# Kernel optimization log

Measured on AMD Instinct MI355X. Metric: run time of the kernel, lower is better.

## Reference

```python
import jax, jax.numpy as jnp
import numpy as np

L = 12      # n_blocks
H = 12      # n_heads
V = 64      # val_dim
D = 768     # hidden_d (token dim)
MLP = 3072  # MLP_dim
NP = 14     # n_patches per side
PS = 16     # patch size
C = 3       # channels
NC = 1000   # num_classes
EPS = 1e-5  # LayerNorm eps


def pos_embeddings(S, d):
    # result[i,j] = sin(i/10000**(j/d)) if j even else cos(i/10000**((j-1)/d))
    i = jnp.arange(S, dtype=jnp.float32)[:, None]
    j = jnp.arange(d, dtype=jnp.float32)[None, :]
    angle = i / jnp.power(10000.0, (j - (j % 2)) / d)
    even = (jnp.arange(d) % 2) == 0
    return jnp.where(even[None, :], jnp.sin(angle), jnp.cos(angle))


def patchify(images):
    # [n,C,H,W] -> [n, NP*NP, C*PS*PS], patch flattened in (c, ph, pw) order
    n = images.shape[0]
    x = images.reshape(n, C, NP, PS, NP, PS)
    x = x.transpose(0, 2, 4, 1, 3, 5)  # n, i, j, c, ps, ps
    return x.reshape(n, NP * NP, C * PS * PS)


def layernorm(x, w, b):
    m = jnp.mean(x, axis=-1, keepdims=True)
    v = jnp.var(x, axis=-1, keepdims=True)
    return (x - m) * jax.lax.rsqrt(v + EPS) * w + b


def setup_inputs() -> dict:
    key = jax.random.key(0)
    ks = jax.random.split(key, 10)
    s = lambda k, shape, scale=0.02: jax.random.normal(k, shape, jnp.float32) * scale
    return {
        "images": jax.random.normal(ks[0], (32, C, NP * PS, NP * PS), jnp.float32),
        "W_map": s(ks[1], (C * PS * PS, D)),          # linear_mapper (no bias)
        "class_token": s(ks[2], (1, D), 1.0),
        "pos_emb": pos_embeddings(NP * NP + 1, D),     # buffer
        "ln1_w": jnp.ones((L, D)), "ln1_b": jnp.zeros((L, D)),
        "qkv_w": s(ks[3], (L, D, 3 * H * V)),          # to_qkv (no bias)
        "merge_w": s(ks[4], (L, H * V, D)),            # Merge (no bias)
        "ln2_w": jnp.ones((L, D)), "ln2_b": jnp.zeros((L, D)),
        "mlp_w1": s(ks[5], (L, D, MLP)), "mlp_b1": jnp.zeros((L, MLP)),
        "mlp_w2": s(ks[6], (L, MLP, D)), "mlp_b2": jnp.zeros((L, D)),
        "head_w": s(ks[7], (D, NC)), "head_b": jnp.zeros((NC,)),
    }


def reference(images, W_map, class_token, pos_emb, ln1_w, ln1_b, qkv_w,
              merge_w, ln2_w, ln2_b, mlp_w1, mlp_b1, mlp_w2, mlp_b2,
              head_w, head_b):
    n = images.shape[0]
    tokens = patchify(images) @ W_map                              # [n, P, D]
    tokens = jnp.concatenate([jnp.broadcast_to(class_token, (n, 1, D)), tokens], axis=1)
    x = tokens + pos_emb                                           # [n, P+1, D]

    def block(x, p):
        l1w, l1b, qw, mw, l2w, l2b, w1, b1, w2, b2 = p
        h = layernorm(x, l1w, l1b)
        # rearrange 'b p (h v k) -> k b h p v' (k innermost factor)
        qkv = (h @ qw).reshape(n, -1, H, V, 3)
        q, k, v = qkv[..., 0], qkv[..., 1], qkv[..., 2]            # [n, P+1, H, V]
        attn = jnp.einsum('bihd,bjhd->bhij', q, k) * (V ** -0.5)
        attn = jax.nn.softmax(attn, axis=-1)
        o = jnp.einsum('bhij,bjhd->bihd', attn, v).reshape(n, -1, H * V)
        x = x + o @ mw
        h2 = layernorm(x, l2w, l2b)
        x = x + (jax.nn.gelu(h2 @ w1 + b1, approximate=False) @ w2 + b2)
        return x, None

    x, _ = jax.lax.scan(block, x, (ln1_w, ln1_b, qkv_w, merge_w,
                                   ln2_w, ln2_b, mlp_w1, mlp_b1, mlp_w2, mlp_b2))
    return jax.nn.softmax(x[:, 0] @ head_w + head_b, axis=-1)      # [n, NC]
```

## Files before the change

### kernel.cpp

```cpp
#include <hip/hip_runtime.h>
#include <math.h>

#define NIMG 32
#define NP2  196
#define PTOK 197
#define DIM  768
#define NH   12
#define VD   64
#define MLPD 3072
#define ROWS (NIMG*PTOK)
#define PROWS (NIMG*NP2)
#define LDK 40
#define PSTR 208
#define BHN (NIMG*NH)

typedef float f32x4 __attribute__((ext_vector_type(4)));
typedef short bf16x8 __attribute__((ext_vector_type(8)));
typedef unsigned short u16x8 __attribute__((ext_vector_type(8)));
typedef unsigned short u16x4 __attribute__((ext_vector_type(4)));

__device__ __forceinline__ unsigned short f2bf(float x) {
    unsigned int u = __float_as_uint(x);
    return (unsigned short)((u + 0x7FFFu + ((u >> 16) & 1u)) >> 16);
}
__device__ __forceinline__ float bfhi(unsigned short h) {
    return __uint_as_float(((unsigned int)h) << 16);
}

__global__ __launch_bounds__(256) void patchify_kernel(const float* __restrict__ img,
                                                       float* __restrict__ out)
{
    int idx = blockIdx.x * 256 + threadIdx.x;
    if (idx >= PROWS * DIM) return;
    int row = idx / DIM, kk = idx % DIM;
    int b = row / NP2, p = row % NP2;
    int i = p / 14, j = p % 14;
    int c = kk >> 8, r = kk & 255;
    int ph = r >> 4, pw = r & 15;
    out[idx] = img[(((size_t)b*3 + c)*224 + i*16 + ph)*224 + j*16 + pw];
}

__global__ __launch_bounds__(256) void class_pos_kernel(const float* __restrict__ ct,
                                                        const float* __restrict__ pos,
                                                        float* __restrict__ x)
{
    int idx = blockIdx.x * 256 + threadIdx.x;
    if (idx >= NIMG * DIM) return;
    int b = idx / DIM, d = idx % DIM;
    x[(size_t)b * PTOK * DIM + d] = ct[d] + pos[d];
}

__device__ __forceinline__ void conv_body(const float* __restrict__ W,
    unsigned short* __restrict__ Bh, unsigned short* __restrict__ Bl, int K, int N)
{
    int idx = blockIdx.x * 256 + threadIdx.x;
    if (idx >= N * (K >> 5)) return;
    int kb = idx / N;
    int n  = idx - kb * N;
    size_t off = (((size_t)(n >> 7) * (K >> 5) + kb) * 128 + (n & 127)) * 32;
    #pragma unroll
    for (int u = 0; u < 4; ++u) {
        u16x8 h, l;
        #pragma unroll
        for (int j = 0; j < 8; ++j) {
            float x = W[(size_t)(kb * 32 + u * 8 + j) * N + n];
            unsigned short hh = f2bf(x);
            h[j] = hh;
            l[j] = f2bf(x - bfhi(hh));
        }
        *(u16x8*)&Bh[off + u * 8] = h;
        *(u16x8*)&Bl[off + u * 8] = l;
    }
}

__global__ __launch_bounds__(256) void convert_one(const float* __restrict__ W,
    unsigned short* __restrict__ Bh, unsigned short* __restrict__ Bl, int K, int N)
{
    conv_body(W, Bh, Bl, K, N);
}

__global__ __launch_bounds__(256) void convert_layer(
    const float* __restrict__ qw, const float* __restrict__ mw,
    const float* __restrict__ w1, const float* __restrict__ w2,
    unsigned short* qh, unsigned short* ql, unsigned short* mh, unsigned short* ml,
    unsigned short* h1, unsigned short* l1, unsigned short* h2, unsigned short* l2)
{
    switch (blockIdx.y) {
        case 0: conv_body(qw, qh, ql, DIM, 3*NH*VD); break;
        case 1: conv_body(mw, mh, ml, DIM, DIM);     break;
        case 2: conv_body(w1, h1, l1, DIM, MLPD);    break;
        case 3: conv_body(w2, h2, l2, MLPD, DIM);    break;
    }
}

template<int MODE>
__global__ __launch_bounds__(256, 2) void mgemm(
    const float* __restrict__ A,
    const unsigned short* __restrict__ Bh, const unsigned short* __restrict__ Bl,
    float* __restrict__ C, int M, int N, int K,
    const float* __restrict__ bias, const float* __restrict__ res,
    const float* __restrict__ pos,
    unsigned int* __restrict__ qo, unsigned int* __restrict__ ko, unsigned int* __restrict__ vo)
{
    __shared__ unsigned short AhS[128 * LDK];
    __shared__ unsigned short AlS[128 * LDK];
    __shared__ unsigned short BhS[128 * LDK];
    __shared__ unsigned short BlS[128 * LDK];

    const int tid = threadIdx.x;
    const int m0 = blockIdx.y * 128, n0 = blockIdx.x * 128;
    const int wave = tid >> 6, lane = tid & 63;
    const int wm = (wave >> 1) * 64, wn = (wave & 1) * 64;
    const int lr = lane & 15, lg = lane >> 4;

    const int ar = tid >> 1, ac = (tid & 1) * 16;
    const bool aok = (m0 + ar) < M;
    const float* aP = A + (size_t)(aok ? (m0 + ar) : 0) * K + ac;
    const size_t bBase = ((size_t)(n0 >> 7) * (K >> 5)) * 4096 + (size_t)tid * 16;
    const unsigned short* bhP = Bh + bBase;
    const unsigned short* blP = Bl + bBase;
    const int wOff = ar * LDK + ac;
    const int aOff = (wm + lr) * LDK + lg * 8;
    const int bOff = (wn + lr) * LDK + lg * 8;

    f32x4 acc[4][4];
    #pragma unroll
    for (int i = 0; i < 4; ++i)
        #pragma unroll
        for (int j = 0; j < 4; ++j)
            #pragma unroll
            for (int e = 0; e < 4; ++e) acc[i][j][e] = 0.f;

    f32x4 avr0, avr1, avr2, avr3;
    u16x8 bhr0, bhr1, blr0, blr1;

#define LOAD_REGS(KS) do { \
    const float* _p = aP + (size_t)(KS) * 32; \
    avr0 = *(const f32x4*)(_p);      avr1 = *(const f32x4*)(_p + 4); \
    avr2 = *(const f32x4*)(_p + 8);  avr3 = *(const f32x4*)(_p + 12); \
    const unsigned short* _ph = bhP + (size_t)(KS) * 4096; \
    const unsigned short* _pl = blP + (size_t)(KS) * 4096; \
    bhr0 = *(const u16x8*)(_ph); bhr1 = *(const u16x8*)(_ph + 8); \
    blr0 = *(const u16x8*)(_pl); blr1 = *(const u16x8*)(_pl + 8); \
} while (0)

    const int kSteps = K >> 5;
    LOAD_REGS(0);

    #pragma unroll 1
    for (int ks = 0; ks < kSteps; ++ks) {
        __syncthreads();
        {
            u16x8 ahv, alv;
            #pragma unroll
            for (int j = 0; j < 4; ++j) {
                unsigned short hh = f2bf(avr0[j]);
                ahv[j] = hh; alv[j] = f2bf(avr0[j] - bfhi(hh));
            }
            #pragma unroll
            for (int j = 0; j < 4; ++j) {
                unsigned short hh = f2bf(avr1[j]);
                ahv[4 + j] = hh; alv[4 + j] = f2bf(avr1[j] - bfhi(hh));
            }
            *(u16x8*)&AhS[wOff] = ahv;
            *(u16x8*)&AlS[wOff] = alv;
            #pragma unroll
            for (int j = 0; j < 4; ++j) {
                unsigned short hh = f2bf(avr2[j]);
                ahv[j] = hh; alv[j] = f2bf(avr2[j] - bfhi(hh));
            }
            #pragma unroll
            for (int j = 0; j < 4; ++j) {
                unsigned short hh = f2bf(avr3[j]);
                ahv[4 + j] = hh; alv[4 + j] = f2bf(avr3[j] - bfhi(hh));
            }
            *(u16x8*)&AhS[wOff + 8] = ahv;
            *(u16x8*)&AlS[wOff + 8] = alv;
            *(u16x8*)&BhS[wOff] = bhr0;
            *(u16x8*)&BhS[wOff + 8] = bhr1;
            *(u16x8*)&BlS[wOff] = blr0;
            *(u16x8*)&BlS[wOff + 8] = blr1;
        }
        __syncthreads();
        if (ks + 1 < kSteps) LOAD_REGS(ks + 1);

        bf16x8 afh[4], afl[4], bfh[4], bfl[4];
        #pragma unroll
        for (int i = 0; i < 4; ++i) {
            afh[i] = *(const bf16x8*)&AhS[aOff + i * (16 * LDK)];
            afl[i] = *(const bf16x8*)&AlS[aOff + i * (16 * LDK)];
            bfh[i] = *(const bf16x8*)&BhS[bOff + i * (16 * LDK)];
            bfl[i] = *(const bf16x8*)&BlS[bOff + i * (16 * LDK)];
        }
        #pragma unroll
        for (int mi = 0; mi < 4; ++mi)
            #pragma unroll
            for (int ni = 0; ni < 4; ++ni) {
                acc[mi][ni] = __builtin_amdgcn_mfma_f32_16x16x32_bf16(afh[mi], bfh[ni], acc[mi][ni], 0, 0, 0);
                acc[mi][ni] = __builtin_amdgcn_mfma_f32_16x16x32_bf16(afh[mi], bfl[ni], acc[mi][ni], 0, 0, 0);
                acc[mi][ni] = __builtin_amdgcn_mfma_f32_16x16x32_bf16(afl[mi], bfh[ni], acc[mi][ni], 0, 0, 0);
            }
    }
#undef LOAD_REGS

    #pragma unroll
    for (int mi = 0; mi < 4; ++mi) {
        #pragma unroll
        for (int ni = 0; ni < 4; ++ni) {
            f32x4 v = acc[mi][ni];
            int c = n0 + wn + ni * 16 + lr;
            #pragma unroll
            for (int rr = 0; rr < 4; ++rr) {
                int r = m0 + wm + mi * 16 + lg * 4 + rr;
                if (r >= M) continue;
                float val = v[rr];
                if (MODE == 1) {
                    int b = r / NP2, p = r - b * NP2;
                    C[((size_t)b * PTOK + 1 + p) * DIM + c] = val + pos[(size_t)(p + 1) * DIM + c];
                } else if (MODE == 2) {
                    int b = r / PTOK, p = r - b * PTOK;
                    int t = c % 3, hv = c / 3;
                    int hd = hv >> 6, vv = hv & 63;
                    size_t bh = (size_t)b * NH + hd;
                    float sv = (t == 0) ? val * 0.125f : val;
                    unsigned short hi = f2bf(sv);
                    unsigned short lo = f2bf(sv - bfhi(hi));
                    unsigned int w32 = (unsigned int)hi | ((unsigned int)lo << 16);
                    if (t == 2) vo[(bh * 64 + vv) * PSTR + p] = w32;
                    else if (t == 0) qo[(bh * PSTR + p) * 64 + vv] = w32;
                    else ko[(bh * PSTR + p) * 64 + vv] = w32;
                } else if (MODE == 3) {
                    float tmp = val + bias[c];
                    C[(size_t)r * N + c] = 0.5f * tmp * (1.0f + erff(tmp * 0.70710678118654752f));
                } else if (MODE == 4) {
                    C[(size_t)r * N + c] = res[(size_t)r * N + c] + val;
                } else if (MODE == 5) {
                    C[(size_t)r * N + c] = res[(size_t)r * N + c] + val + bias[c];
                }
            }
        }
    }
}

__global__ __launch_bounds__(256) void ln_kernel(const float* __restrict__ x,
                                                 const float* __restrict__ w,
                                                 const float* __restrict__ b,
                                                 float* __restrict__ out, int rows)
{
    int wave = threadIdx.x >> 6, lane = threadIdx.x & 63;
    int row = blockIdx.x * 4 + wave;
    if (row >= rows) return;
    const float* xr = x + (size_t)row * DIM;
    float vals[12];
    float sum = 0.f;
    #pragma unroll
    for (int u = 0; u < 12; ++u) { vals[u] = xr[u * 64 + lane]; sum += vals[u]; }
    #pragma unroll
    for (int off = 32; off; off >>= 1) sum += __shfl_xor(sum, off);
    float mean = sum * (1.f / DIM);
    float vs = 0.f;
    #pragma unroll
    for (int u = 0; u < 12; ++u) { float d = vals[u] - mean; vs += d * d; }
    #pragma unroll
    for (int off = 32; off; off >>= 1) vs += __shfl_xor(vs, off);
    float rstd = rsqrtf(vs * (1.f / DIM) + 1e-5f);
    float* orow = out + (size_t)row * DIM;
    #pragma unroll
    for (int u = 0; u < 12; ++u) {
        int d = u * 64 + lane;
        orow[d] = (vals[u] - mean) * rstd * w[d] + b[d];
    }
}

__global__ __launch_bounds__(256) void attn_mfma(
    const unsigned int* __restrict__ qp, const unsigned int* __restrict__ kp,
    const unsigned int* __restrict__ vtp, float* __restrict__ og)
{
    __shared__ unsigned short KVh[64 * 72];
    __shared__ unsigned short KVl[64 * 72];
    __shared__ unsigned short Ph[64 * 72];
    __shared__ unsigned short Pl[64 * 72];

    const int tid = threadIdx.x;
    const int w = tid >> 6, lane = tid & 63;
    const int l = lane & 15, g = lane >> 4;
    const int bh = blockIdx.y, q0 = blockIdx.x * 64;
    const int b = bh / NH, hd = bh - b * NH;

    int qrow = q0 + 16 * w + l;
    if (qrow >= PTOK) qrow = 0;
    const unsigned int* qbase = qp + ((size_t)bh * PSTR + qrow) * 64;
    bf16x8 qAh[2], qAl[2];
    #pragma unroll
    for (int ks = 0; ks < 2; ++ks) {
        const unsigned int* p = qbase + 32 * ks + 8 * g;
        uint4 a = *(const uint4*)p;
        uint4 c = *(const uint4*)(p + 4);
        bf16x8 h8, l8;
        h8[0]=(short)a.x; h8[1]=(short)a.y; h8[2]=(short)a.z; h8[3]=(short)a.w;
        h8[4]=(short)c.x; h8[5]=(short)c.y; h8[6]=(short)c.z; h8[7]=(short)c.w;
        l8[0]=(short)(a.x>>16); l8[1]=(short)(a.y>>16); l8[2]=(short)(a.z>>16); l8[3]=(short)(a.w>>16);
        l8[4]=(short)(c.x>>16); l8[5]=(short)(c.y>>16); l8[6]=(short)(c.z>>16); l8[7]=(short)(c.w>>16);
        qAh[ks] = h8; qAl[ks] = l8;
    }

    f32x4 s[13];
    #pragma unroll
    for (int t = 0; t < 13; ++t)
        #pragma unroll
        for (int e = 0; e < 4; ++e) s[t][e] = 0.f;

    for (int c = 0; c < 4; ++c) {
        __syncthreads();
        const int rows = (c < 3) ? 64 : 16;
        for (int u = tid; u < rows * 16; u += 256) {
            int r = u >> 4, cc = u & 15;
            int j = c * 64 + r;
            uint4 wv = make_uint4(0, 0, 0, 0);
            if (j < PTOK) wv = *(const uint4*)(kp + ((size_t)bh * PSTR + j) * 64 + cc * 4);
            u16x4 h4, l4;
            h4[0]=(unsigned short)wv.x; h4[1]=(unsigned short)wv.y;
            h4[2]=(unsigned short)wv.z; h4[3]=(unsigned short)wv.w;
            l4[0]=(unsigned short)(wv.x>>16); l4[1]=(unsigned short)(wv.y>>16);
            l4[2]=(unsigned short)(wv.z>>16); l4[3]=(unsigned short)(wv.w>>16);
            *(u16x4*)&KVh[r * 72 + cc * 4] = h4;
            *(u16x4*)&KVl[r * 72 + cc * 4] = l4;
        }
        __syncthreads();
        const int tc = (c < 3) ? 4 : 1;
        for (int t = 0; t < tc; ++t) {
            int ti = c * 4 + t;
            #pragma unroll
            for (int ks = 0; ks < 2; ++ks) {
                bf16x8 kh = *(const bf16x8*)&KVh[(16 * t + l) * 72 + 32 * ks + 8 * g];
                bf16x8 kl = *(const bf16x8*)&KVl[(16 * t + l) * 72 + 32 * ks + 8 * g];
                s[ti] = __builtin_amdgcn_mfma_f32_16x16x32_bf16(qAh[ks], kh, s[ti], 0, 0, 0);
                s[ti] = __builtin_amdgcn_mfma_f32_16x16x32_bf16(qAh[ks], kl, s[ti], 0, 0, 0);
                s[ti] = __builtin_amdgcn_mfma_f32_16x16x32_bf16(qAl[ks], kh, s[ti], 0, 0, 0);
            }
        }
    }

    if (l >= 5) {
        #pragma unroll
        for (int e = 0; e < 4; ++e) s[12][e] = -1e30f;
    }

    float mx[4], rs[4];
    #pragma unroll
    for (int e = 0; e < 4; ++e) {
        float m = s[0][e];
        #pragma unroll
        for (int t = 1; t < 13; ++t) m = fmaxf(m, s[t][e]);
        #pragma unroll
        for (int off = 1; off < 16; off <<= 1) m = fmaxf(m, __shfl_xor(m, off));
        mx[e] = m;
    }
    #pragma unroll
    for (int e = 0; e < 4; ++e) {
        float sum = 0.f;
        #pragma unroll
        for (int t = 0; t < 13; ++t) {
            float p = __expf(s[t][e] - mx[e]);
            s[t][e] = p;
            sum += p;
        }
        #pragma unroll
        for (int off = 1; off < 16; off <<= 1) sum += __shfl_xor(sum, off);
        rs[e] = 1.f / sum;
    }

    f32x4 o[4];
    #pragma unroll
    for (int t = 0; t < 4; ++t)
        #pragma unroll
        for (int e = 0; e < 4; ++e) o[t][e] = 0.f;

    for (int c = 0; c < 4; ++c) {
        __syncthreads();
        const int cols = (c < 3) ? 64 : 32;
        const int cpr = cols >> 2;
        for (int u = tid; u < 64 * cpr; u += 256) {
            int r = u / cpr, cc = u % cpr;
            int jbase = c * 64 + cc * 4;
            uint4 wv;
            if (c < 3) {
                wv = *(const uint4*)(vtp + ((size_t)bh * 64 + r) * PSTR + jbase);
            } else {
                unsigned int t0 = (jbase + 0 < PTOK) ? vtp[((size_t)bh * 64 + r) * PSTR + jbase + 0] : 0u;
                unsigned int t1 = (jbase + 1 < PTOK) ? vtp[((size_t)bh * 64 + r) * PSTR + jbase + 1] : 0u;
                unsigned int t2 = (jbase + 2 < PTOK) ? vtp[((size_t)bh * 64 + r) * PSTR + jbase + 2] : 0u;
                unsigned int t3 = (jbase + 3 < PTOK) ? vtp[((size_t)bh * 64 + r) * PSTR + jbase + 3] : 0u;
                wv = make_uint4(t0, t1, t2, t3);
            }
            u16x4 h4, l4;
            h4[0]=(unsigned short)wv.x; h4[1]=(unsigned short)wv.y;
            h4[2]=(unsigned short)wv.z; h4[3]=(unsigned short)wv.w;
            l4[0]=(unsigned short)(wv.x>>16); l4[1]=(unsigned short)(wv.y>>16);
            l4[2]=(unsigned short)(wv.z>>16); l4[3]=(unsigned short)(wv.w>>16);
            *(u16x4*)&KVh[r * 72 + cc * 4] = h4;
            *(u16x4*)&KVl[r * 72 + cc * 4] = l4;
        }
        const int tc = (c < 3) ? 4 : 1;
        for (int t = 0; t < tc; ++t) {
            int ti = c * 4 + t;
            #pragma unroll
            for (int e = 0; e < 4; ++e) {
                int row = 16 * w + 4 * g + e, col = 16 * t + l;
                float pv = s[ti][e];
                unsigned short hi = f2bf(pv);
                Ph[row * 72 + col] = hi;
                Pl[row * 72 + col] = f2bf(pv - bfhi(hi));
            }
        }
        __syncthreads();
        const int ksn = (c < 3) ? 2 : 1;
        for (int ks = 0; ks < ksn; ++ks) {
            bf16x8 pa_h = *(const bf16x8*)&Ph[(16 * w + l) * 72 + 32 * ks + 8 * g];
            bf16x8 pa_l = *(const bf16x8*)&Pl[(16 * w + l) * 72 + 32 * ks + 8 * g];
            #pragma unroll
            for (int tv = 0; tv < 4; ++tv) {
                bf16x8 vh = *(const bf16x8*)&KVh[(16 * tv + l) * 72 + 32 * ks + 8 * g];
                bf16x8 vl = *(const bf16x8*)&KVl[(16 * tv + l) * 72 + 32 * ks + 8 * g];
                o[tv] = __builtin_amdgcn_mfma_f32_16x16x32_bf16(pa_h, vh, o[tv], 0, 0, 0);
                o[tv] = __builtin_amdgcn_mfma_f32_16x16x32_bf16(pa_h, vl, o[tv], 0, 0, 0);
                o[tv] = __builtin_amdgcn_mfma_f32_16x16x32_bf16(pa_l, vh, o[tv], 0, 0, 0);
            }
        }
    }

    #pragma unroll
    for (int tv = 0; tv < 4; ++tv) {
        #pragma unroll
        for (int e = 0; e < 4; ++e) {
            int q = q0 + 16 * w + 4 * g + e;
            if (q < PTOK)
                og[((size_t)(b * PTOK + q)) * DIM + hd * 64 + 16 * tv + l] = o[tv][e] * rs[e];
        }
    }
}

__global__ __launch_bounds__(256) void head_kernel(const float* __restrict__ x,
                                                   const float* __restrict__ W,
                                                   const float* __restrict__ bias,
                                                   float* __restrict__ out)
{
    __shared__ __align__(16) float xl[DIM];
    __shared__ float red[4];
    int b = blockIdx.x;
    const float* xr = x + (size_t)b * PTOK * DIM;
    for (int idx = threadIdx.x; idx < DIM; idx += 256) xl[idx] = xr[idx];
    __syncthreads();

    float logit[4];
    #pragma unroll
    for (int u = 0; u < 4; ++u) {
        int c = threadIdx.x + u * 256;
        float acc = (c < 1000) ? bias[c] : -INFINITY;
        if (c < 1000) {
            for (int k = 0; k < DIM; k += 4) {
                float4 xv = *(const float4*)&xl[k];
                acc += xv.x * W[(size_t)k * 1000 + c]
                     + xv.y * W[(size_t)(k + 1) * 1000 + c]
                     + xv.z * W[(size_t)(k + 2) * 1000 + c]
                     + xv.w * W[(size_t)(k + 3) * 1000 + c];
            }
        }
        logit[u] = acc;
    }
    int lane = threadIdx.x & 63, wv = threadIdx.x >> 6;
    float m = fmaxf(fmaxf(logit[0], logit[1]), fmaxf(logit[2], logit[3]));
    #pragma unroll
    for (int off = 32; off; off >>= 1) m = fmaxf(m, __shfl_xor(m, off));
    if (lane == 0) red[wv] = m;
    __syncthreads();
    m = fmaxf(fmaxf(red[0], red[1]), fmaxf(red[2], red[3]));

    float p[4]; float sum = 0.f;
    #pragma unroll
    for (int u = 0; u < 4; ++u) {
        int c = threadIdx.x + u * 256;
        p[u] = (c < 1000) ? expf(logit[u] - m) : 0.f;
        sum += p[u];
    }
    #pragma unroll
    for (int off = 32; off; off >>= 1) sum += __shfl_xor(sum, off);
    __syncthreads();
    if (lane == 0) red[wv] = sum;
    __syncthreads();
    float inv = 1.f / (red[0] + red[1] + red[2] + red[3]);
    #pragma unroll
    for (int u = 0; u < 4; ++u) {
        int c = threadIdx.x + u * 256;
        if (c < 1000) out[(size_t)b * 1000 + c] = p[u] * inv;
    }
}

extern "C" void kernel_launch(void* const* d_in, const int* in_sizes, int n_in,
                              void* d_out, int out_size, void* d_ws, size_t ws_size,
                              hipStream_t stream)
{
    const float* images  = (const float*)d_in[0];
    const float* W_map   = (const float*)d_in[1];
    const float* ct      = (const float*)d_in[2];
    const float* pos     = (const float*)d_in[3];
    const float* ln1_w   = (const float*)d_in[4];
    const float* ln1_b   = (const float*)d_in[5];
    const float* qkv_w   = (const float*)d_in[6];
    const float* merge_w = (const float*)d_in[7];
    const float* ln2_w   = (const float*)d_in[8];
    const float* ln2_b   = (const float*)d_in[9];
    const float* mlp_w1  = (const float*)d_in[10];
    const float* mlp_b1  = (const float*)d_in[11];
    const float* mlp_w2  = (const float*)d_in[12];
    const float* mlp_b2  = (const float*)d_in[13];
    const float* head_w  = (const float*)d_in[14];
    const float* head_b  = (const float*)d_in[15];
    float* out = (float*)d_out;

    float* ws = (float*)d_ws;
    const size_t XE = (size_t)ROWS * DIM;
    float* x  = ws;
    float* h  = x  + XE;
    float* ob = h  + XE;
    float* g  = ob + XE;

    const size_t PL = (size_t)BHN * PSTR * 64;
    unsigned int* qpl = (unsigned int*)g;
    unsigned int* kpl = qpl + PL;
    unsigned int* vtp = kpl + PL;
    float* patches = g;

    unsigned short* wb = (unsigned short*)(g + (size_t)ROWS * MLPD);
    const size_t qkvE = (size_t)DIM * 2304;
    const size_t mgE  = (size_t)DIM * DIM;
    const size_t m1E  = (size_t)DIM * MLPD;
    const size_t m2E  = (size_t)MLPD * DIM;
    unsigned short* qh  = wb;
    unsigned short* ql  = qh  + qkvE;
    unsigned short* mh  = ql  + qkvE;
    unsigned short* ml  = mh  + mgE;
    unsigned short* h1  = ml  + mgE;
    unsigned short* l1  = h1  + m1E;
    unsigned short* h2  = l1  + m1E;
    unsigned short* l2  = h2  + m2E;
    unsigned short* wmh = l2  + m2E;
    unsigned short* wml = wmh + mgE;

    patchify_kernel<<<(PROWS * DIM + 255) / 256, 256, 0, stream>>>(images, patches);
    class_pos_kernel<<<(NIMG * DIM + 255) / 256, 256, 0, stream>>>(ct, pos, x);
    convert_one<<<(DIM * (DIM / 32) + 255) / 256, 256, 0, stream>>>(W_map, wmh, wml, DIM, DIM);
    mgemm<1><<<dim3(DIM / 128, PROWS / 128), 256, 0, stream>>>(
        patches, wmh, wml, x, PROWS, DIM, DIM, nullptr, nullptr, pos, nullptr, nullptr, nullptr);

    const int mblk = (ROWS + 127) / 128;
    for (int l = 0; l < 12; ++l) {
        convert_layer<<<dim3(288, 4), 256, 0, stream>>>(
            qkv_w + (size_t)l * qkvE, merge_w + (size_t)l * mgE,
            mlp_w1 + (size_t)l * m1E, mlp_w2 + (size_t)l * m2E,
            qh, ql, mh, ml, h1, l1, h2, l2);
        ln_kernel<<<(ROWS + 3) / 4, 256, 0, stream>>>(x, ln1_w + l * DIM, ln1_b + l * DIM, h, ROWS);
        mgemm<2><<<dim3(2304 / 128, mblk), 256, 0, stream>>>(
            h, qh, ql, nullptr, ROWS, 2304, DIM, nullptr, nullptr, nullptr, qpl, kpl, vtp);
        attn_mfma<<<dim3(4, BHN), 256, 0, stream>>>(qpl, kpl, vtp, ob);
        mgemm<4><<<dim3(DIM / 128, mblk), 256, 0, stream>>>(
            ob, mh, ml, x, ROWS, DIM, DIM, nullptr, x, nullptr, nullptr, nullptr, nullptr);
        ln_kernel<<<(ROWS + 3) / 4, 256, 0, stream>>>(x, ln2_w + l * DIM, ln2_b + l * DIM, h, ROWS);
        mgemm<3><<<dim3(MLPD / 128, mblk), 256, 0, stream>>>(
            h, h1, l1, g, ROWS, MLPD, DIM, mlp_b1 + (size_t)l * MLPD, nullptr, nullptr, nullptr, nullptr, nullptr);
        mgemm<5><<<dim3(DIM / 128, mblk), 256, 0, stream>>>(
            g, h2, l2, x, ROWS, DIM, MLPD, mlp_b2 + (size_t)l * DIM, x, nullptr, nullptr, nullptr, nullptr);
    }
    head_kernel<<<NIMG, 256, 0, stream>>>(x, head_w, head_b, out);
}
```

Measured before the change: 6.436 ms.

## Pre-split activations into bf16 hi/lo planes and stream GEMM tiles via global_load_lds

Producers (patchify, layernorm, attention output, GELU epilogue) now write activations as bf16 hi/lo pairs instead of fp32, so the GEMM no longer converts A in its inner loop. The GEMM loads both A and B tiles directly into XOR-swizzled shared memory with global_load_lds, drops register staging and padding, raises launch bounds to 3 blocks, and swaps the grid axes so M-tiles vary fastest. The aim is less per-k-step ALU and register pressure and higher occupancy. In exchange the GEMM loses its register prefetch of the next tile, so loads are no longer overlapped with the MFMAs, and rows beyond M rely on padded MPAD buffers with no bounds check.

```diff
diff --git a/kernel.cpp b/kernel.cpp
--- a/kernel.cpp
+++ b/kernel.cpp
@@ -10,7 +10,7 @@
 #define MLPD 3072
 #define ROWS (NIMG*PTOK)
 #define PROWS (NIMG*NP2)
-#define LDK 40
+#define MPAD 6400
 #define PSTR 208
 #define BHN (NIMG*NH)
 
@@ -26,9 +26,15 @@
 __device__ __forceinline__ float bfhi(unsigned short h) {
     return __uint_as_float(((unsigned int)h) << 16);
 }
+__device__ __forceinline__ void glds16(const unsigned short* g, unsigned short* l) {
+    __builtin_amdgcn_global_load_lds(
+        (const __attribute__((address_space(1))) unsigned int*)g,
+        (__attribute__((address_space(3))) unsigned int*)l, 16, 0, 0);
+}
 
 __global__ __launch_bounds__(256) void patchify_kernel(const float* __restrict__ img,
-                                                       float* __restrict__ out)
+                                                       unsigned short* __restrict__ ph,
+                                                       unsigned short* __restrict__ pl)
 {
     int idx = blockIdx.x * 256 + threadIdx.x;
     if (idx >= PROWS * DIM) return;
@@ -36,8 +42,11 @@
     int b = row / NP2, p = row % NP2;
     int i = p / 14, j = p % 14;
     int c = kk >> 8, r = kk & 255;
-    int ph = r >> 4, pw = r & 15;
-    out[idx] = img[(((size_t)b*3 + c)*224 + i*16 + ph)*224 + j*16 + pw];
+    int pr = r >> 4, pw = r & 15;
+    float v = img[(((size_t)b*3 + c)*224 + i*16 + pr)*224 + j*16 + pw];
+    unsigned short hi = f2bf(v);
+    ph[idx] = hi;
+    pl[idx] = f2bf(v - bfhi(hi));
 }
 
 __global__ __launch_bounds__(256) void class_pos_kernel(const float* __restrict__ ct,
@@ -94,34 +103,43 @@
 }
 
 template<int MODE>
-__global__ __launch_bounds__(256, 2) void mgemm(
-    const float* __restrict__ A,
+__global__ __launch_bounds__(256, 3) void mgemm(
+    const unsigned short* __restrict__ Ah, const unsigned short* __restrict__ Al,
     const unsigned short* __restrict__ Bh, const unsigned short* __restrict__ Bl,
     float* __restrict__ C, int M, int N, int K,
     const float* __restrict__ bias, const float* __restrict__ res,
     const float* __restrict__ pos,
-    unsigned int* __restrict__ qo, unsigned int* __restrict__ ko, unsigned int* __restrict__ vo)
-{
-    __shared__ unsigned short AhS[128 * LDK];
-    __shared__ unsigned short AlS[128 * LDK];
-    __shared__ unsigned short BhS[128 * LDK];
-    __shared__ unsigned short BlS[128 * LDK];
+    unsigned int* __restrict__ qo, unsigned int* __restrict__ ko, unsigned int* __restrict__ vo,
+    unsigned short* __restrict__ oph, unsigned short* __restrict__ opl)
+{
+    __shared__ unsigned short SAh[128 * 32];
+    __shared__ unsigned short SAl[128 * 32];
+    __shared__ unsigned short SBh[128 * 32];
+    __shared__ unsigned short SBl[128 * 32];
 
     const int tid = threadIdx.x;
-    const int m0 = blockIdx.y * 128, n0 = blockIdx.x * 128;
+    const int m0 = blockIdx.x * 128, n0 = blockIdx.y * 128;
     const int wave = tid >> 6, lane = tid & 63;
     const int wm = (wave >> 1) * 64, wn = (wave & 1) * 64;
     const int lr = lane & 15, lg = lane >> 4;
 
-    const int ar = tid >> 1, ac = (tid & 1) * 16;
-    const bool aok = (m0 + ar) < M;
-    const float* aP = A + (size_t)(aok ? (m0 + ar) : 0) * K + ac;
-    const size_t bBase = ((size_t)(n0 >> 7) * (K >> 5)) * 4096 + (size_t)tid * 16;
-    const unsigned short* bhP = Bh + bBase;
-    const unsigned short* blP = Bl + bBase;
-    const int wOff = ar * LDK + ac;
-    const int aOff = (wm + lr) * LDK + lg * 8;
-    const int bOff = (wn + lr) * LDK + lg * 8;
+    const int r0 = tid >> 2, sl = tid & 3;
+    const int s0 = sl ^ ((r0 >> 1) & 3);
+    const size_t aoff0 = (size_t)(m0 + r0) * K + s0 * 8;
+    const size_t aoff1 = (size_t)(m0 + r0 + 64) * K + s0 * 8;
+    const size_t boff0 = (size_t)(n0 >> 7) * (K >> 5) * 4096 + (size_t)r0 * 32 + s0 * 8;
+    const size_t boff1 = boff0 + 64 * 32;
+    unsigned short* dst0 = (unsigned short*)((char*)nullptr);
+    (void)dst0;
+
+    int aro[4], bro[4];
+    #pragma unroll
+    for (int i = 0; i < 4; ++i) {
+        int rowA = wm + i * 16 + lr;
+        aro[i] = rowA * 32 + ((lg ^ ((rowA >> 1) & 3)) * 8);
+        int rowB = wn + i * 16 + lr;
+        bro[i] = rowB * 32 + ((lg ^ ((rowB >> 1) & 3)) * 8);
+    }
 
     f32x4 acc[4][4];
     #pragma unroll
@@ -131,77 +149,40 @@
             #pragma unroll
             for (int e = 0; e < 4; ++e) acc[i][j][e] = 0.f;
 
-    f32x4 avr0, avr1, avr2, avr3;
-    u16x8 bhr0, bhr1, blr0, blr1;
-
-#define LOAD_REGS(KS) do { \
-    const float* _p = aP + (size_t)(KS) * 32; \
-    avr0 = *(const f32x4*)(_p);      avr1 = *(const f32x4*)(_p + 4); \
-    avr2 = *(const f32x4*)(_p + 8);  avr3 = *(const f32x4*)(_p + 12); \
-    const unsigned short* _ph = bhP + (size_t)(KS) * 4096; \
-    const unsigned short* _pl = blP + (size_t)(KS) * 4096; \
-    bhr0 = *(const u16x8*)(_ph); bhr1 = *(const u16x8*)(_ph + 8); \
-    blr0 = *(const u16x8*)(_pl); blr1 = *(const u16x8*)(_pl + 8); \
-} while (0)
-
     const int kSteps = K >> 5;
-    LOAD_REGS(0);
-
     #pragma unroll 1
     for (int ks = 0; ks < kSteps; ++ks) {
         __syncthreads();
-        {
-            u16x8 ahv, alv;
-            #pragma unroll
-            for (int j = 0; j < 4; ++j) {
-                unsigned short hh = f2bf(avr0[j]);
-                ahv[j] = hh; alv[j] = f2bf(avr0[j] - bfhi(hh));
-            }
-            #pragma unroll
-            for (int j = 0; j < 4; ++j) {
-                unsigned short hh = f2bf(avr1[j]);
-                ahv[4 + j] = hh; alv[4 + j] = f2bf(avr1[j] - bfhi(hh));
-            }
-            *(u16x8*)&AhS[wOff] = ahv;
-            *(u16x8*)&AlS[wOff] = alv;
-            #pragma unroll
-            for (int j = 0; j < 4; ++j) {
-                unsigned short hh = f2bf(avr2[j]);
-                ahv[j] = hh; alv[j] = f2bf(avr2[j] - bfhi(hh));
-            }
-            #pragma unroll
-            for (int j = 0; j < 4; ++j) {
-                unsigned short hh = f2bf(avr3[j]);
-                ahv[4 + j] = hh; alv[4 + j] = f2bf(avr3[j] - bfhi(hh));
-            }
-            *(u16x8*)&AhS[wOff + 8] = ahv;
-            *(u16x8*)&AlS[wOff + 8] = alv;
-            *(u16x8*)&BhS[wOff] = bhr0;
-            *(u16x8*)&BhS[wOff + 8] = bhr1;
-            *(u16x8*)&BlS[wOff] = blr0;
-            *(u16x8*)&BlS[wOff + 8] = blr1;
-        }
+        const size_t ak = (size_t)ks * 32;
+        const size_t bk = (size_t)ks * 4096;
+        glds16(Ah + aoff0 + ak, SAh + tid * 8);
+        glds16(Ah + aoff1 + ak, SAh + 2048 + tid * 8);
+        glds16(Al + aoff0 + ak, SAl + tid * 8);
+        glds16(Al + aoff1 + ak, SAl + 2048 + tid * 8);
+        glds16(Bh + boff0 + bk, SBh + tid * 8);
+        glds16(Bh + boff1 + bk, SBh + 2048 + tid * 8);
+        glds16(Bl + boff0 + bk, SBl + tid * 8);
+        glds16(Bl + boff1 + bk, SBl + 2048 + tid * 8);
         __syncthreads();
-        if (ks + 1 < kSteps) LOAD_REGS(ks + 1);
-
-        bf16x8 afh[4], afl[4], bfh[4], bfl[4];
-        #pragma unroll
-        for (int i = 0; i < 4; ++i) {
-            afh[i] = *(const bf16x8*)&AhS[aOff + i * (16 * LDK)];
-            afl[i] = *(const bf16x8*)&AlS[aOff + i * (16 * LDK)];
-            bfh[i] = *(const bf16x8*)&BhS[bOff + i * (16 * LDK)];
-            bfl[i] = *(const bf16x8*)&BlS[bOff + i * (16 * LDK)];
-        }
-        #pragma unroll
-        for (int mi = 0; mi < 4; ++mi)
+
+        bf16x8 bfh[4], bfl[4];
+        #pragma unroll
+        for (int ni = 0; ni < 4; ++ni) {
+            bfh[ni] = *(const bf16x8*)&SBh[bro[ni]];
+            bfl[ni] = *(const bf16x8*)&SBl[bro[ni]];
+        }
+        #pragma unroll
+        for (int mi = 0; mi < 4; ++mi) {
+            bf16x8 afh = *(const bf16x8*)&SAh[aro[mi]];
+            bf16x8 afl = *(const bf16x8*)&SAl[aro[mi]];
             #pragma unroll
             for (int ni = 0; ni < 4; ++ni) {
-                acc[mi][ni] = __builtin_amdgcn_mfma_f32_16x16x32_bf16(afh[mi], bfh[ni], acc[mi][ni], 0, 0, 0);
-                acc[mi][ni] = __builtin_amdgcn_mfma_f32_16x16x32_bf16(afh[mi], bfl[ni], acc[mi][ni], 0, 0, 0);
-                acc[mi][ni] = __builtin_amdgcn_mfma_f32_16x16x32_bf16(afl[mi], bfh[ni], acc[mi][ni], 0, 0, 0);
-            }
-    }
-#undef LOAD_REGS
+                acc[mi][ni] = __builtin_amdgcn_mfma_f32_16x16x32_bf16(afh, bfh[ni], acc[mi][ni], 0, 0, 0);
+                acc[mi][ni] = __builtin_amdgcn_mfma_f32_16x16x32_bf16(afh, bfl[ni], acc[mi][ni], 0, 0, 0);
+                acc[mi][ni] = __builtin_amdgcn_mfma_f32_16x16x32_bf16(afl, bfh[ni], acc[mi][ni], 0, 0, 0);
+            }
+        }
+    }
 
     #pragma unroll
     for (int mi = 0; mi < 4; ++mi) {
@@ -231,7 +212,10 @@
                     else ko[(bh * PSTR + p) * 64 + vv] = w32;
                 } else if (MODE == 3) {
                     float tmp = val + bias[c];
-                    C[(size_t)r * N + c] = 0.5f * tmp * (1.0f + erff(tmp * 0.70710678118654752f));
+                    float gel = 0.5f * tmp * (1.0f + erff(tmp * 0.70710678118654752f));
+                    unsigned short hi = f2bf(gel);
+                    oph[(size_t)r * N + c] = hi;
+                    opl[(size_t)r * N + c] = f2bf(gel - bfhi(hi));
                 } else if (MODE == 4) {
                     C[(size_t)r * N + c] = res[(size_t)r * N + c] + val;
                 } else if (MODE == 5) {
@@ -245,7 +229,8 @@
 __global__ __launch_bounds__(256) void ln_kernel(const float* __restrict__ x,
                                                  const float* __restrict__ w,
                                                  const float* __restrict__ b,
-                                                 float* __restrict__ out, int rows)
+                                                 unsigned short* __restrict__ oh,
+                                                 unsigned short* __restrict__ ol, int rows)
 {
     int wave = threadIdx.x >> 6, lane = threadIdx.x & 63;
     int row = blockIdx.x * 4 + wave;
@@ -264,17 +249,20 @@
     #pragma unroll
     for (int off = 32; off; off >>= 1) vs += __shfl_xor(vs, off);
     float rstd = rsqrtf(vs * (1.f / DIM) + 1e-5f);
-    float* orow = out + (size_t)row * DIM;
     #pragma unroll
     for (int u = 0; u < 12; ++u) {
         int d = u * 64 + lane;
-        orow[d] = (vals[u] - mean) * rstd * w[d] + b[d];
+        float v = (vals[u] - mean) * rstd * w[d] + b[d];
+        unsigned short hi = f2bf(v);
+        oh[(size_t)row * DIM + d] = hi;
+        ol[(size_t)row * DIM + d] = f2bf(v - bfhi(hi));
     }
 }
 
 __global__ __launch_bounds__(256) void attn_mfma(
     const unsigned int* __restrict__ qp, const unsigned int* __restrict__ kp,
-    const unsigned int* __restrict__ vtp, float* __restrict__ og)
+    const unsigned int* __restrict__ vtp,
+    unsigned short* __restrict__ oh, unsigned short* __restrict__ ol)
 {
     __shared__ unsigned short KVh[64 * 72];
     __shared__ unsigned short KVl[64 * 72];
@@ -434,8 +422,13 @@
         #pragma unroll
         for (int e = 0; e < 4; ++e) {
             int q = q0 + 16 * w + 4 * g + e;
-            if (q < PTOK)
-                og[((size_t)(b * PTOK + q)) * DIM + hd * 64 + 16 * tv + l] = o[tv][e] * rs[e];
+            if (q < PTOK) {
+                float v = o[tv][e] * rs[e];
+                size_t idx = ((size_t)(b * PTOK + q)) * DIM + hd * 64 + 16 * tv + l;
+                unsigned short hi = f2bf(v);
+                oh[idx] = hi;
+                ol[idx] = f2bf(v - bfhi(hi));
+            }
         }
     }
 }
@@ -519,19 +512,26 @@
     float* out = (float*)d_out;
 
     float* ws = (float*)d_ws;
-    const size_t XE = (size_t)ROWS * DIM;
-    float* x  = ws;
-    float* h  = x  + XE;
-    float* ob = h  + XE;
-    float* g  = ob + XE;
+    const size_t XE   = (size_t)ROWS * DIM;
+    const size_t PLND = (size_t)MPAD * DIM;
+    const size_t GPL  = (size_t)MPAD * MLPD;
+
+    float* x = ws;
+    unsigned short* hh = (unsigned short*)(x + XE);
+    unsigned short* hl = hh + PLND;
+    unsigned short* oh = hl + PLND;
+    unsigned short* ol = oh + PLND;
+    unsigned short* gh = ol + PLND;
+    unsigned short* gl = gh + GPL;
 
     const size_t PL = (size_t)BHN * PSTR * 64;
-    unsigned int* qpl = (unsigned int*)g;
+    unsigned int* qpl = (unsigned int*)gh;
     unsigned int* kpl = qpl + PL;
     unsigned int* vtp = kpl + PL;
-    float* patches = g;
-
-    unsigned short* wb = (unsigned short*)(g + (size_t)ROWS * MLPD);
+    unsigned short* pph = gh;
+    unsigned short* ppl = pph + (size_t)PROWS * DIM;
+
+    unsigned short* wb = gl + GPL;
     const size_t qkvE = (size_t)DIM * 2304;
     const size_t mgE  = (size_t)DIM * DIM;
     const size_t m1E  = (size_t)DIM * MLPD;
@@ -547,29 +547,34 @@
     unsigned short* wmh = l2  + m2E;
     unsigned short* wml = wmh + mgE;
 
-    patchify_kernel<<<(PROWS * DIM + 255) / 256, 256, 0, stream>>>(images, patches);
+    patchify_kernel<<<(PROWS * DIM + 255) / 256, 256, 0, stream>>>(images, pph, ppl);
     class_pos_kernel<<<(NIMG * DIM + 255) / 256, 256, 0, stream>>>(ct, pos, x);
     convert_one<<<(DIM * (DIM / 32) + 255) / 256, 256, 0, stream>>>(W_map, wmh, wml, DIM, DIM);
-    mgemm<1><<<dim3(DIM / 128, PROWS / 128), 256, 0, stream>>>(
-        patches, wmh, wml, x, PROWS, DIM, DIM, nullptr, nullptr, pos, nullptr, nullptr, nullptr);
-
-    const int mblk = (ROWS + 127) / 128;
+    mgemm<1><<<dim3(PROWS / 128, DIM / 128), 256, 0, stream>>>(
+        pph, ppl, wmh, wml, x, PROWS, DIM, DIM,
+        nullptr, nullptr, pos, nullptr, nullptr, nullptr, nullptr, nullptr);
+
+    const int gm = (ROWS + 127) / 128;
     for (int l = 0; l < 12; ++l) {
         convert_layer<<<dim3(288, 4), 256, 0, stream>>>(
             qkv_w + (size_t)l * qkvE, merge_w + (size_t)l * mgE,
             mlp_w1 + (size_t)l * m1E, mlp_w2 + (size_t)l * m2E,
             qh, ql, mh, ml, h1, l1, h2, l2);
-        ln_kernel<<<(ROWS + 3) / 4, 256, 0, stream>>>(x, ln1_w + l * DIM, ln1_b + l * DIM, h, ROWS);
-        mgemm<2><<<dim3(2304 / 128, mblk), 256, 0, stream>>>(
-            h, qh, ql, nullptr, ROWS, 2304, DIM, nullptr, nullptr, nullptr, qpl, kpl, vtp);
-        attn_mfma<<<dim3(4, BHN), 256, 0, stream>>>(qpl, kpl, vtp, ob);
-        mgemm<4><<<dim3(DIM / 128, mblk), 256, 0, stream>>>(
-            ob, mh, ml, x, ROWS, DIM, DIM, nullptr, x, nullptr, nullptr, nullptr, nullptr);
-        ln_kernel<<<(ROWS + 3) / 4, 256, 0, stream>>>(x, ln2_w + l * DIM, ln2_b + l * DIM, h, ROWS);
-        mgemm<3><<<dim3(MLPD / 128, mblk), 256, 0, stream>>>(
-            h, h1, l1, g, ROWS, MLPD, DIM, mlp_b1 + (size_t)l * MLPD, nullptr, nullptr, nullptr, nullptr, nullptr);
-        mgemm<5><<<dim3(DIM / 128, mblk), 256, 0, stream>>>(
-            g, h2, l2, x, ROWS, DIM, MLPD, mlp_b2 + (size_t)l * DIM, x, nullptr, nullptr, nullptr, nullptr);
+        ln_kernel<<<(ROWS + 3) / 4, 256, 0, stream>>>(x, ln1_w + l * DIM, ln1_b + l * DIM, hh, hl, ROWS);
+        mgemm<2><<<dim3(gm, 2304 / 128), 256, 0, stream>>>(
+            hh, hl, qh, ql, nullptr, ROWS, 2304, DIM,
+            nullptr, nullptr, nullptr, qpl, kpl, vtp, nullptr, nullptr);
+        attn_mfma<<<dim3(4, BHN), 256, 0, stream>>>(qpl, kpl, vtp, oh, ol);
+        mgemm<4><<<dim3(gm, DIM / 128), 256, 0, stream>>>(
+            oh, ol, mh, ml, x, ROWS, DIM, DIM,
+            nullptr, x, nullptr, nullptr, nullptr, nullptr, nullptr, nullptr);
+        ln_kernel<<<(ROWS + 3) / 4, 256, 0, stream>>>(x, ln2_w + l * DIM, ln2_b + l * DIM, hh, hl, ROWS);
+        mgemm<3><<<dim3(gm, MLPD / 128), 256, 0, stream>>>(
+            hh, hl, h1, l1, nullptr, ROWS, MLPD, DIM,
+            mlp_b1 + (size_t)l * MLPD, nullptr, nullptr, nullptr, nullptr, nullptr, gh, gl);
+        mgemm<5><<<dim3(gm, DIM / 128), 256, 0, stream>>>(
+            gh, gl, h2, l2, x, ROWS, DIM, MLPD,
+            mlp_b2 + (size_t)l * DIM, x, nullptr, nullptr, nullptr, nullptr, nullptr, nullptr);
     }
     head_kernel<<<NIMG, 256, 0, stream>>>(x, head_w, head_b, out);
 }
```

New measurement: 5.901 ms. 1.09x faster.
